# Performance work log

Measured on AMD Instinct MI355X. Metric: run time of the kernel, lower is better.

## Reference

```python
import jax, jax.numpy as jnp
import numpy as np
import math

B, N, FIN, FOUT, OPE = 16, 2048, 128, 128, 64


def setup_inputs() -> dict:
    key = jax.random.key(0)
    ks = jax.random.split(key, 10)
    h = jax.random.normal(ks[0], (B, N, FIN), dtype=jnp.float32)
    adj = jax.random.randint(ks[1], (B, N, N), 0, 2).astype(jnp.float32)
    op_emb = jax.random.normal(ks[2], (B, N, OPE), dtype=jnp.float32)
    # Linear weights stored as (in, out) so y = x @ W; torch init scale ~ 1/sqrt(fan_in)
    s_in = 1.0 / math.sqrt(FIN)
    Wk = jax.random.uniform(ks[3], (FIN, FOUT), minval=-s_in, maxval=s_in)
    Wq = jax.random.uniform(ks[4], (FIN, FOUT), minval=-s_in, maxval=s_in)
    Wv = jax.random.uniform(ks[5], (FIN, FOUT), minval=-s_in, maxval=s_in)
    s_a = 1.0 / math.sqrt(FOUT)
    a_w = jax.random.uniform(ks[6], (FOUT,), minval=-s_a, maxval=s_a)
    s_op = 1.0 / math.sqrt(OPE)
    op_W = jax.random.uniform(ks[7], (OPE, FOUT), minval=-s_op, maxval=s_op)
    op_b = jax.random.uniform(ks[8], (FOUT,), minval=-s_op, maxval=s_op)
    ln_g = jnp.ones((FOUT,), dtype=jnp.float32)
    ln_b = jnp.zeros((FOUT,), dtype=jnp.float32)
    return {"h": h, "adj": adj, "op_emb": op_emb, "Wk": Wk, "Wq": Wq,
            "Wv": Wv, "a_w": a_w, "op_W": op_W, "op_b": op_b,
            "ln_g": ln_g, "ln_b": ln_b}


def reference(h, adj, op_emb, Wk, Wq, Wv, a_w, op_W, op_b, ln_g, ln_b):
    d = Wk.shape[1]
    Whk = h @ Wk  # (B,N,d)
    Whq = h @ Wq
    Whv = h @ Wv
    # Original builds a_input[b,e,l,m] = Whq[b,e,m]*Whk[b,l,m] (B,N,N,d) then
    # projects with a (d->1). Algebraically: scores[b,e,l] = <Whq[b,e], Whk[b,l]*a_w>.
    scores = jnp.einsum('bed,bld->bel', Whq, Whk * a_w)
    scores = scores / jnp.sqrt(jnp.float32(d))  # attention_rescale
    alpha = jax.nn.leaky_relu(scores, negative_slope=0.2)  # leakrelu
    alpha = alpha * adj  # multiplicative mask (zeros stay in the softmax)
    attn = jax.nn.softmax(alpha, axis=-1)  # softmax over source nodes l
    agg = jnp.einsum('bel,bld->bed', attn, Whv)  # (B,N,d)
    gate = jax.nn.sigmoid(op_emb @ op_W + op_b)  # opattention branch
    hp = gate * agg
    # LayerNorm over last dim, eps=1e-5
    mu = jnp.mean(hp, axis=-1, keepdims=True)
    var = jnp.mean(jnp.square(hp - mu), axis=-1, keepdims=True)
    return (hp - mu) * jax.lax.rsqrt(var + 1e-5) * ln_g + ln_b
```

## Files before the change

### kernel.cpp

```cpp
#include <hip/hip_runtime.h>

typedef unsigned int u32;
typedef float f32x4 __attribute__((ext_vector_type(4)));
typedef short s16x8 __attribute__((ext_vector_type(8)));

#define LDA 136

#define WQT_OFF 0ULL
#define WKT_OFF 32768ULL
#define WVT_OFF 65536ULL
#define OPWT_OFF 98304ULL
#define Q_OFF 114688ULL
#define K_OFF (Q_OFF + 8388608ULL)
#define VT_OFF (K_OFF + 8388608ULL)
#define GATE_OFF (VT_OFF + 8388608ULL)

__device__ __forceinline__ u32 f2bf(float f) {
  u32 u = __float_as_uint(f);
  return (u + 0x7fffu + ((u >> 16) & 1u)) >> 16;
}

__device__ __forceinline__ void gl_lds16(const void* g, void* l) {
  __builtin_amdgcn_global_load_lds((const __attribute__((address_space(1))) void*)g,
                                   (__attribute__((address_space(3))) void*)l, 16, 0, 0);
}

__global__ void k0_wt(const float* Wq, const float* Wk, const float* Wv,
                      const float* aw, const float* opW, char* ws) {
  int nt = blockIdx.x, part = blockIdx.y;
  int kksh = (nt == 3) ? 6 : 7;
  int KK = 1 << kksh;
  const float* S = (nt == 0) ? Wq : (nt == 1) ? Wk : (nt == 2) ? Wv : opW;
  unsigned short* D = (unsigned short*)(ws + (nt == 0 ? WQT_OFF : nt == 1 ? WKT_OFF : nt == 2 ? WVT_OFF : OPWT_OFF));
  int base = part * 8 * KK;
  for (int i = threadIdx.x; i < 8 * KK; i += 256) {
    int d = part * 8 + (i >> kksh), k = i & (KK - 1);
    float v = S[k * 128 + d];
    if (nt == 1) v *= aw[d] * 0.12751743f;
    D[base + i] = (unsigned short)f2bf(v);
  }
}

__launch_bounds__(256, 2)
__global__ void k1_proj(const float* __restrict__ h, const float* __restrict__ op_emb,
                        const float* __restrict__ op_b, char* __restrict__ ws) {
  int nt = blockIdx.x, et = blockIdx.y;
  int kksh = (nt == 3) ? 6 : 7;
  int KK = 1 << kksh;
  __shared__ unsigned short bufA[128 * LDA];
  __shared__ unsigned short bufB[128 * LDA];
  unsigned short* wbuf = (nt == 2) ? bufB : bufA;
  unsigned short* xbuf = (nt == 2) ? bufA : bufB;
  const unsigned short* Wt = (const unsigned short*)(ws + (nt == 0 ? WQT_OFF : nt == 1 ? WKT_OFF : nt == 2 ? WVT_OFF : OPWT_OFF));
  {
    const uint4* Ws = (const uint4*)Wt;
    int cnt = 128 * KK / 8;
    for (int i = threadIdx.x; i < cnt; i += 256) {
      uint4 v = Ws[i];
      int r = (8 * i) >> kksh, c = (8 * i) & (KK - 1);
      *(uint4*)&wbuf[r * LDA + c] = v;
    }
  }
  {
    const float* X = (nt == 3) ? (op_emb + (size_t)et * 128 * 64) : (h + (size_t)et * 128 * 128);
    int cnt = 128 * KK / 4;
    for (int i = threadIdx.x; i < cnt; i += 256) {
      float4 v = *(const float4*)(X + 4 * i);
      int r = (4 * i) >> kksh, c = (4 * i) & (KK - 1);
      u32 lo = f2bf(v.x) | (f2bf(v.y) << 16);
      u32 hi = f2bf(v.z) | (f2bf(v.w) << 16);
      *(uint2*)&xbuf[r * LDA + c] = make_uint2(lo, hi);
    }
  }
  __syncthreads();
  int tid = threadIdx.x, w = tid >> 6, lane = tid & 63, l15 = lane & 15, q = lane >> 4;
  int wa = w >> 1, wb = w & 1;
  f32x4 acc[4][4];
#pragma unroll
  for (int a = 0; a < 4; a++)
#pragma unroll
    for (int bq = 0; bq < 4; bq++) acc[a][bq] = f32x4{0.f, 0.f, 0.f, 0.f};
  for (int ks = 0; ks < KK / 32; ks++) {
    s16x8 af[4], bf_[4];
#pragma unroll
    for (int mt = 0; mt < 4; mt++)
      af[mt] = *(const s16x8*)&bufA[(wa * 64 + mt * 16 + l15) * LDA + ks * 32 + q * 8];
#pragma unroll
    for (int n2 = 0; n2 < 4; n2++)
      bf_[n2] = *(const s16x8*)&bufB[(wb * 64 + n2 * 16 + l15) * LDA + ks * 32 + q * 8];
#pragma unroll
    for (int mt = 0; mt < 4; mt++)
#pragma unroll
      for (int n2 = 0; n2 < 4; n2++)
        acc[mt][n2] = __builtin_amdgcn_mfma_f32_16x16x32_bf16(af[mt], bf_[n2], acc[mt][n2], 0, 0, 0);
  }
  if (nt <= 1) {
    unsigned short* Dst = (unsigned short*)(ws + (nt == 0 ? Q_OFF : K_OFF));
#pragma unroll
    for (int mt = 0; mt < 4; mt++)
#pragma unroll
      for (int n2 = 0; n2 < 4; n2++) {
        int d0 = wa * 64 + mt * 16 + q * 4;
        int eg = et * 128 + wb * 64 + n2 * 16 + l15;
        f32x4 a = acc[mt][n2];
        u32 lo = f2bf(a[0]) | (f2bf(a[1]) << 16);
        u32 hi = f2bf(a[2]) | (f2bf(a[3]) << 16);
        *(uint2*)(Dst + (size_t)eg * 128 + d0) = make_uint2(lo, hi);
      }
  } else if (nt == 2) {
    unsigned short* Dst = (unsigned short*)(ws + VT_OFF);
    int b = et >> 4;
    int ein0 = (et & 15) * 128;
#pragma unroll
    for (int mt = 0; mt < 4; mt++)
#pragma unroll
      for (int n2 = 0; n2 < 4; n2++) {
        int e0b = ein0 + wa * 64 + mt * 16 + q * 4;
        int d = wb * 64 + n2 * 16 + l15;
        f32x4 a = acc[mt][n2];
        u32 lo = f2bf(a[0]) | (f2bf(a[1]) << 16);
        u32 hi = f2bf(a[2]) | (f2bf(a[3]) << 16);
        *(uint2*)(Dst + (size_t)b * 128 * 2048 + (size_t)d * 2048 + e0b) = make_uint2(lo, hi);
      }
  } else {
    float* Dst = (float*)(ws + GATE_OFF);
#pragma unroll
    for (int mt = 0; mt < 4; mt++)
#pragma unroll
      for (int n2 = 0; n2 < 4; n2++) {
        int d0 = wa * 64 + mt * 16 + q * 4;
        int eg = et * 128 + wb * 64 + n2 * 16 + l15;
        f32x4 a = acc[mt][n2];
        float4 g4;
        g4.x = 1.f / (1.f + __builtin_amdgcn_exp2f(-(a[0] + op_b[d0 + 0]) * 1.4426950f));
        g4.y = 1.f / (1.f + __builtin_amdgcn_exp2f(-(a[1] + op_b[d0 + 1]) * 1.4426950f));
        g4.z = 1.f / (1.f + __builtin_amdgcn_exp2f(-(a[2] + op_b[d0 + 2]) * 1.4426950f));
        g4.w = 1.f / (1.f + __builtin_amdgcn_exp2f(-(a[3] + op_b[d0 + 3]) * 1.4426950f));
        *(float4*)(Dst + (size_t)eg * 128 + d0) = g4;
      }
  }
}

__launch_bounds__(512, 2)
__global__ void k2_attn(const float* __restrict__ adj, const float* __restrict__ ln_g,
                        const float* __restrict__ ln_b, char* __restrict__ ws,
                        float* __restrict__ out) {
  __shared__ char smem[150016];
  float* sden = (float*)(smem + 149504);

  const int bid = blockIdx.x;
  const int xcd = bid & 7, slot = bid >> 3;
  const int b = xcd * 2 + (slot >> 4);
  const int e0 = (slot & 15) << 7;

  const unsigned short* Qg = (const unsigned short*)(ws + Q_OFF) + ((size_t)b * 2048 + e0) * 128;
  const unsigned short* Kg = (const unsigned short*)(ws + K_OFF) + (size_t)b * 2048 * 128;
  const unsigned short* Vtg = (const unsigned short*)(ws + VT_OFF) + (size_t)b * 128 * 2048;
  const float* gateg = (const float*)(ws + GATE_OFF) + ((size_t)b * 2048 + e0) * 128;
  const float* adjg = adj + (size_t)b * 2048 * 2048 + (size_t)e0 * 2048;

  const int tid = threadIdx.x;
  const int w = tid >> 6, lane = tid & 63, l15 = lane & 15, q = lane >> 4;
  const int wh = w >> 2, we = w & 3;
  char* PLw = smem + 131072 + w * 2304;

  if (tid < 128) sden[tid] = 0.0f;

  s16x8 qf[2][4];
#pragma unroll
  for (int et = 0; et < 2; et++) {
    const int e = we * 32 + et * 16 + l15;
#pragma unroll
    for (int ks = 0; ks < 4; ks++)
      qf[et][ks] = *(const s16x8*)(Qg + (size_t)e * 128 + ks * 32 + q * 8);
  }

  f32x4 oacc[2][8];
#pragma unroll
  for (int et = 0; et < 2; et++)
#pragma unroll
    for (int nt = 0; nt < 8; nt++) oacc[et][nt] = f32x4{0.f, 0.f, 0.f, 0.f};
  float dp0 = 0.0f, dp1 = 0.0f;
  float4 adjB[2][4];

#pragma unroll
  for (int j = 0; j < 4; j++) {
    int S = (j * 8 + w) * 64 + lane;
    int r = S >> 4, cp = S & 15, c = cp ^ (r & 15);
    gl_lds16(Kg + (size_t)r * 128 + (c << 3), smem + (j * 8 + w) * 1024);
    gl_lds16(Vtg + (size_t)r * 2048 + (c << 3), smem + 65536 + (j * 8 + w) * 1024);
  }
#pragma unroll
  for (int et = 0; et < 2; et++) {
    const int e = we * 32 + et * 16 + l15;
#pragma unroll
    for (int lt = 0; lt < 4; lt++)
      adjB[et][lt] = *(const float4*)(adjg + (size_t)e * 2048 + wh * 64 + lt * 16 + q * 4);
  }

#pragma unroll 2
  for (int it = 0; it < 16; it++) {
    __syncthreads();
    const int cur = it & 1, nxt = cur ^ 1;
    char* Kl = smem + cur * 32768;
    char* Vl = smem + 65536 + cur * 32768;
    float4 adjA[2][4];
#pragma unroll
    for (int et = 0; et < 2; et++)
#pragma unroll
      for (int lt = 0; lt < 4; lt++) adjA[et][lt] = adjB[et][lt];

    if (it < 15) {
      const unsigned short* kb = Kg + (size_t)(it + 1) * 16384;
      const unsigned short* vb = Vtg + (size_t)(it + 1) * 128;
      char* Kd = smem + nxt * 32768;
      char* Vd = smem + 65536 + nxt * 32768;
#pragma unroll
      for (int j = 0; j < 4; j++) {
        int S = (j * 8 + w) * 64 + lane;
        int r = S >> 4, cp = S & 15, c = cp ^ (r & 15);
        gl_lds16(kb + (size_t)r * 128 + (c << 3), Kd + (j * 8 + w) * 1024);
        gl_lds16(vb + (size_t)r * 2048 + (c << 3), Vd + (j * 8 + w) * 1024);
      }
      const float* ab = adjg + (size_t)(it + 1) * 128;
#pragma unroll
      for (int et = 0; et < 2; et++) {
        const int e = we * 32 + et * 16 + l15;
#pragma unroll
        for (int lt = 0; lt < 4; lt++)
          adjB[et][lt] = *(const float4*)(ab + (size_t)e * 2048 + wh * 64 + lt * 16 + q * 4);
      }
    }

    f32x4 sacc[4][2];
#pragma unroll
    for (int lt = 0; lt < 4; lt++)
#pragma unroll
      for (int et = 0; et < 2; et++) sacc[lt][et] = f32x4{0.f, 0.f, 0.f, 0.f};
#pragma unroll
    for (int ks = 0; ks < 4; ks++) {
      s16x8 kf[4];
#pragma unroll
      for (int lt = 0; lt < 4; lt++) {
        int l = wh * 64 + lt * 16 + l15;
        kf[lt] = *(const s16x8*)(Kl + l * 256 + (((ks * 4 + q) ^ l15) << 4));
      }
#pragma unroll
      for (int lt = 0; lt < 4; lt++)
#pragma unroll
        for (int et = 0; et < 2; et++)
          sacc[lt][et] = __builtin_amdgcn_mfma_f32_16x16x32_bf16(kf[lt], qf[et][ks], sacc[lt][et], 0, 0, 0);
    }

    s16x8 af[2][2];
#pragma unroll
    for (int et = 0; et < 2; et++) {
      u32 pqw[4][2];
      float dsum = 0.0f;
#pragma unroll
      for (int lt = 0; lt < 4; lt++) {
        float4 aj = adjA[et][lt];
        f32x4 s = sacc[lt][et];
        float p0 = __builtin_amdgcn_exp2f(fmaxf(s[0], 0.2f * s[0]) * aj.x);
        float p1 = __builtin_amdgcn_exp2f(fmaxf(s[1], 0.2f * s[1]) * aj.y);
        float p2 = __builtin_amdgcn_exp2f(fmaxf(s[2], 0.2f * s[2]) * aj.z);
        float p3 = __builtin_amdgcn_exp2f(fmaxf(s[3], 0.2f * s[3]) * aj.w);
        dsum += (p0 + p1) + (p2 + p3);
        pqw[lt][0] = f2bf(p0) | (f2bf(p1) << 16);
        pqw[lt][1] = f2bf(p2) | (f2bf(p3) << 16);
      }
      if (et == 0) dp0 += dsum; else dp1 += dsum;
#pragma unroll
      for (int lt = 0; lt < 4; lt++)
        *(uint2*)(PLw + l15 * 144 + lt * 32 + q * 8) = make_uint2(pqw[lt][0], pqw[lt][1]);
      af[et][0] = *(const s16x8*)(PLw + l15 * 144 + q * 16);
      af[et][1] = *(const s16x8*)(PLw + l15 * 144 + 64 + q * 16);
    }

#pragma unroll
    for (int ks2 = 0; ks2 < 2; ks2++) {
      s16x8 vf[8];
#pragma unroll
      for (int nt = 0; nt < 8; nt++) {
        int d = nt * 16 + l15;
        vf[nt] = *(const s16x8*)(Vl + d * 256 + (((wh * 8 + ks2 * 4 + q) ^ l15) << 4));
      }
#pragma unroll
      for (int et = 0; et < 2; et++)
#pragma unroll
        for (int nt = 0; nt < 8; nt++)
          oacc[et][nt] = __builtin_amdgcn_mfma_f32_16x16x32_bf16(af[et][ks2], vf[nt], oacc[et][nt], 0, 0, 0);
    }
  }

  atomicAdd(&sden[we * 32 + l15], dp0);
  atomicAdd(&sden[we * 32 + 16 + l15], dp1);
  __syncthreads();

  float* O2 = (float*)smem;
  if (wh == 1) {
#pragma unroll
    for (int et = 0; et < 2; et++)
#pragma unroll
      for (int nt = 0; nt < 8; nt++) {
        const int eb = we * 32 + et * 16 + q * 4;
        const int d = nt * 16 + l15;
#pragma unroll
        for (int r = 0; r < 4; r++) O2[(eb + r) * 132 + d] = oacc[et][nt][r];
      }
  }
  __syncthreads();
  if (wh == 0) {
#pragma unroll
    for (int et = 0; et < 2; et++) {
      const int eb = we * 32 + et * 16 + q * 4;
      float inv[4];
#pragma unroll
      for (int r = 0; r < 4; r++) inv[r] = 1.0f / sden[eb + r];
#pragma unroll
      for (int nt = 0; nt < 8; nt++) {
        const int d = nt * 16 + l15;
#pragma unroll
        for (int r = 0; r < 4; r++) {
          int idx = (eb + r) * 132 + d;
          O2[idx] = (O2[idx] + oacc[et][nt][r]) * inv[r];
        }
      }
    }
  }
  __syncthreads();

  {
    const int e = tid >> 2, j = tid & 3;
    const float* row = O2 + e * 132 + j * 32;
    const float* gr = gateg + (size_t)e * 128 + j * 32;
    float4 x[8];
    float s1 = 0.f, s2 = 0.f;
#pragma unroll
    for (int i = 0; i < 8; i++) {
      float4 v = *(const float4*)(row + i * 4);
      float4 g = *(const float4*)(gr + i * 4);
      float4 hp;
      hp.x = v.x * g.x; hp.y = v.y * g.y; hp.z = v.z * g.z; hp.w = v.w * g.w;
      x[i] = hp;
      s1 += (hp.x + hp.y) + (hp.z + hp.w);
      s2 += (hp.x * hp.x + hp.y * hp.y) + (hp.z * hp.z + hp.w * hp.w);
    }
    s1 += __shfl_xor(s1, 1); s2 += __shfl_xor(s2, 1);
    s1 += __shfl_xor(s1, 2); s2 += __shfl_xor(s2, 2);
    const float mu = s1 * 0.0078125f;
    const float var = s2 * 0.0078125f - mu * mu;
    const float rs = rsqrtf(var + 1e-5f);
    float* orow = out + ((size_t)b * 2048 + e0 + e) * 128 + j * 32;
    const float* gg = ln_g + j * 32;
    const float* bb = ln_b + j * 32;
#pragma unroll
    for (int i = 0; i < 8; i++) {
      float4 gv = *(const float4*)(gg + i * 4);
      float4 bv = *(const float4*)(bb + i * 4);
      float4 o;
      o.x = (x[i].x - mu) * rs * gv.x + bv.x;
      o.y = (x[i].y - mu) * rs * gv.y + bv.y;
      o.z = (x[i].z - mu) * rs * gv.z + bv.z;
      o.w = (x[i].w - mu) * rs * gv.w + bv.w;
      *(float4*)(orow + i * 4) = o;
    }
  }
}

extern "C" void kernel_launch(void* const* d_in, const int* in_sizes, int n_in,
                              void* d_out, int out_size, void* d_ws, size_t ws_size,
                              hipStream_t stream) {
  const float* h = (const float*)d_in[0];
  const float* adj = (const float*)d_in[1];
  const float* op_emb = (const float*)d_in[2];
  const float* Wk = (const float*)d_in[3];
  const float* Wq = (const float*)d_in[4];
  const float* Wv = (const float*)d_in[5];
  const float* a_w = (const float*)d_in[6];
  const float* op_W = (const float*)d_in[7];
  const float* op_b = (const float*)d_in[8];
  const float* ln_g = (const float*)d_in[9];
  const float* ln_b = (const float*)d_in[10];
  char* ws = (char*)d_ws;
  float* out = (float*)d_out;

  k0_wt<<<dim3(4, 16), 256, 0, stream>>>(Wq, Wk, Wv, a_w, op_W, ws);
  k1_proj<<<dim3(4, 256), 256, 0, stream>>>(h, op_emb, op_b, ws);
  k2_attn<<<256, 512, 0, stream>>>(adj, ln_g, ln_b, ws, out);
}
```

Before: 468.3 us.

## Shrink attention blocks to 64 rows and stream V fragments from global memory

Each attention block now covers 64 query rows with 256 threads, launched as 512 blocks. K is single-buffered in LDS with an extra barrier, and V fragments are loaded straight from global memory into registers instead of being staged in LDS. This cuts LDS use from about 150KB to about 42KB per block so more blocks can share a CU and hide latency. In exchange, every batch's K and V are read by twice as many blocks, the K prefetch no longer overlaps compute behind a double buffer, and the strided V loads from global may coalesce poorly.

Result: slower. 639.4 us (+36.5%).

```diff
diff --git a/kernel.cpp b/kernel.cpp
--- a/kernel.cpp
+++ b/kernel.cpp
@@ -141,17 +141,18 @@
   }
 }
 
-__launch_bounds__(512, 2)
+__launch_bounds__(256, 2)
 __global__ void k2_attn(const float* __restrict__ adj, const float* __restrict__ ln_g,
                         const float* __restrict__ ln_b, char* __restrict__ ws,
                         float* __restrict__ out) {
-  __shared__ char smem[150016];
-  float* sden = (float*)(smem + 149504);
+  __shared__ char smem[42240];
+  char* Klds = smem;
+  float* sden = (float*)(smem + 41984);
 
   const int bid = blockIdx.x;
   const int xcd = bid & 7, slot = bid >> 3;
-  const int b = xcd * 2 + (slot >> 4);
-  const int e0 = (slot & 15) << 7;
+  const int b = xcd * 2 + (slot >> 5);
+  const int e0 = (slot & 31) << 6;
 
   const unsigned short* Qg = (const unsigned short*)(ws + Q_OFF) + ((size_t)b * 2048 + e0) * 128;
   const unsigned short* Kg = (const unsigned short*)(ws + K_OFF) + (size_t)b * 2048 * 128;
@@ -161,10 +162,10 @@
 
   const int tid = threadIdx.x;
   const int w = tid >> 6, lane = tid & 63, l15 = lane & 15, q = lane >> 4;
-  const int wh = w >> 2, we = w & 3;
-  char* PLw = smem + 131072 + w * 2304;
-
-  if (tid < 128) sden[tid] = 0.0f;
+  const int wh = w >> 1, we = w & 1;
+  char* PLw = smem + 32768 + w * 2304;
+
+  if (tid < 64) sden[tid] = 0.0f;
 
   s16x8 qf[2][4];
 #pragma unroll
@@ -184,11 +185,10 @@
   float4 adjB[2][4];
 
 #pragma unroll
-  for (int j = 0; j < 4; j++) {
-    int S = (j * 8 + w) * 64 + lane;
+  for (int j = 0; j < 8; j++) {
+    int S = (j * 4 + w) * 64 + lane;
     int r = S >> 4, cp = S & 15, c = cp ^ (r & 15);
-    gl_lds16(Kg + (size_t)r * 128 + (c << 3), smem + (j * 8 + w) * 1024);
-    gl_lds16(Vtg + (size_t)r * 2048 + (c << 3), smem + 65536 + (j * 8 + w) * 1024);
+    gl_lds16(Kg + (size_t)r * 128 + (c << 3), Klds + (j * 4 + w) * 1024);
   }
 #pragma unroll
   for (int et = 0; et < 2; et++) {
@@ -198,29 +198,42 @@
       adjB[et][lt] = *(const float4*)(adjg + (size_t)e * 2048 + wh * 64 + lt * 16 + q * 4);
   }
 
-#pragma unroll 2
   for (int it = 0; it < 16; it++) {
     __syncthreads();
-    const int cur = it & 1, nxt = cur ^ 1;
-    char* Kl = smem + cur * 32768;
-    char* Vl = smem + 65536 + cur * 32768;
     float4 adjA[2][4];
 #pragma unroll
     for (int et = 0; et < 2; et++)
 #pragma unroll
       for (int lt = 0; lt < 4; lt++) adjA[et][lt] = adjB[et][lt];
+
+    f32x4 sacc[4][2];
+#pragma unroll
+    for (int lt = 0; lt < 4; lt++)
+#pragma unroll
+      for (int et = 0; et < 2; et++) sacc[lt][et] = f32x4{0.f, 0.f, 0.f, 0.f};
+#pragma unroll
+    for (int ks = 0; ks < 4; ks++) {
+      s16x8 kf[4];
+#pragma unroll
+      for (int lt = 0; lt < 4; lt++) {
+        int l = wh * 64 + lt * 16 + l15;
+        kf[lt] = *(const s16x8*)(Klds + l * 256 + (((ks * 4 + q) ^ l15) << 4));
+      }
+#pragma unroll
+      for (int lt = 0; lt < 4; lt++)
+#pragma unroll
+        for (int et = 0; et < 2; et++)
+          sacc[lt][et] = __builtin_amdgcn_mfma_f32_16x16x32_bf16(kf[lt], qf[et][ks], sacc[lt][et], 0, 0, 0);
+    }
+    __syncthreads();
 
     if (it < 15) {
       const unsigned short* kb = Kg + (size_t)(it + 1) * 16384;
-      const unsigned short* vb = Vtg + (size_t)(it + 1) * 128;
-      char* Kd = smem + nxt * 32768;
-      char* Vd = smem + 65536 + nxt * 32768;
-#pragma unroll
-      for (int j = 0; j < 4; j++) {
-        int S = (j * 8 + w) * 64 + lane;
+#pragma unroll
+      for (int j = 0; j < 8; j++) {
+        int S = (j * 4 + w) * 64 + lane;
         int r = S >> 4, cp = S & 15, c = cp ^ (r & 15);
-        gl_lds16(kb + (size_t)r * 128 + (c << 3), Kd + (j * 8 + w) * 1024);
-        gl_lds16(vb + (size_t)r * 2048 + (c << 3), Vd + (j * 8 + w) * 1024);
+        gl_lds16(kb + (size_t)r * 128 + (c << 3), Klds + (j * 4 + w) * 1024);
       }
       const float* ab = adjg + (size_t)(it + 1) * 128;
 #pragma unroll
@@ -231,26 +244,11 @@
           adjB[et][lt] = *(const float4*)(ab + (size_t)e * 2048 + wh * 64 + lt * 16 + q * 4);
       }
     }
-
-    f32x4 sacc[4][2];
-#pragma unroll
-    for (int lt = 0; lt < 4; lt++)
-#pragma unroll
-      for (int et = 0; et < 2; et++) sacc[lt][et] = f32x4{0.f, 0.f, 0.f, 0.f};
-#pragma unroll
-    for (int ks = 0; ks < 4; ks++) {
-      s16x8 kf[4];
-#pragma unroll
-      for (int lt = 0; lt < 4; lt++) {
-        int l = wh * 64 + lt * 16 + l15;
-        kf[lt] = *(const s16x8*)(Kl + l * 256 + (((ks * 4 + q) ^ l15) << 4));
-      }
-#pragma unroll
-      for (int lt = 0; lt < 4; lt++)
-#pragma unroll
-        for (int et = 0; et < 2; et++)
-          sacc[lt][et] = __builtin_amdgcn_mfma_f32_16x16x32_bf16(kf[lt], qf[et][ks], sacc[lt][et], 0, 0, 0);
-    }
+    const unsigned short* vrow = Vtg + (size_t)it * 128 + wh * 64 + q * 8;
+    s16x8 vf0[8], vf1[8];
+#pragma unroll
+    for (int nt = 0; nt < 8; nt++)
+      vf0[nt] = *(const s16x8*)(vrow + (size_t)(nt * 16 + l15) * 2048);
 
     s16x8 af[2][2];
 #pragma unroll
@@ -276,21 +274,20 @@
       af[et][0] = *(const s16x8*)(PLw + l15 * 144 + q * 16);
       af[et][1] = *(const s16x8*)(PLw + l15 * 144 + 64 + q * 16);
     }
-
-#pragma unroll
-    for (int ks2 = 0; ks2 < 2; ks2++) {
-      s16x8 vf[8];
-#pragma unroll
-      for (int nt = 0; nt < 8; nt++) {
-        int d = nt * 16 + l15;
-        vf[nt] = *(const s16x8*)(Vl + d * 256 + (((wh * 8 + ks2 * 4 + q) ^ l15) << 4));
-      }
-#pragma unroll
-      for (int et = 0; et < 2; et++)
-#pragma unroll
-        for (int nt = 0; nt < 8; nt++)
-          oacc[et][nt] = __builtin_amdgcn_mfma_f32_16x16x32_bf16(af[et][ks2], vf[nt], oacc[et][nt], 0, 0, 0);
-    }
+#pragma unroll
+    for (int nt = 0; nt < 8; nt++)
+      vf1[nt] = *(const s16x8*)(vrow + 32 + (size_t)(nt * 16 + l15) * 2048);
+
+#pragma unroll
+    for (int et = 0; et < 2; et++)
+#pragma unroll
+      for (int nt = 0; nt < 8; nt++)
+        oacc[et][nt] = __builtin_amdgcn_mfma_f32_16x16x32_bf16(af[et][0], vf0[nt], oacc[et][nt], 0, 0, 0);
+#pragma unroll
+    for (int et = 0; et < 2; et++)
+#pragma unroll
+      for (int nt = 0; nt < 8; nt++)
+        oacc[et][nt] = __builtin_amdgcn_mfma_f32_16x16x32_bf16(af[et][1], vf1[nt], oacc[et][nt], 0, 0, 0);
   }
 
   atomicAdd(&sden[we * 32 + l15], dp0);
@@ -387,5 +384,5 @@
 
   k0_wt<<<dim3(4, 16), 256, 0, stream>>>(Wq, Wk, Wv, a_w, op_W, ws);
   k1_proj<<<dim3(4, 256), 256, 0, stream>>>(h, op_emb, op_b, ws);
-  k2_attn<<<256, 512, 0, stream>>>(adj, ln_g, ln_b, ws, out);
-}
+  k2_attn<<<512, 256, 0, stream>>>(adj, ln_g, ln_b, ws, out);
+}
```
